# Kernel optimization log

Measured on AMD Instinct MI355X. Metric: run time of the kernel, lower is better.

Reference implementation:

```python
import jax, jax.numpy as jnp
import numpy as np


def setup_inputs() -> dict:
    key = jax.random.key(0)
    B, S, H, D = 4, 2048, 16, 64
    kq, kk, kv, kl = jax.random.split(key, 4)
    q = jax.random.normal(kq, (B, S, H, D), dtype=jnp.float32)
    k = jax.random.normal(kk, (B, S, H, D), dtype=jnp.float32)
    v = jax.random.normal(kv, (B, S, H, D), dtype=jnp.float32)
    # varlen: each sequence has a valid prefix length in [S//2, S]
    lengths = jax.random.randint(kl, (B,), S // 2, S + 1)
    key_padding_mask = jnp.arange(S)[None, :] < lengths[:, None]  # [B, S] bool
    return {"q": q, "k": k, "v": v, "key_padding_mask": key_padding_mask}


def reference(q, k, v, key_padding_mask):
    # q,k,v: [B, S, H, D]; key_padding_mask: [B, S] (True = valid key/value token).
    # Equivalent math of ring varlen flash attention: every query attends to all
    # valid (unpadded) key positions of its sequence; padded keys are excluded.
    D = q.shape[-1]
    scale = 1.0 / np.sqrt(D).astype(np.float32)
    scores = jnp.einsum('bshd,bthd->bhst', q, k) * scale  # [B, H, S, S]
    neg = jnp.finfo(scores.dtype).min
    scores = jnp.where(key_padding_mask[:, None, None, :], scores, neg)
    probs = jax.nn.softmax(scores, axis=-1)
    context = jnp.einsum('bhst,bthd->bshd', probs, v)  # [B, S, H, D]
    return context
```

## Files before the change

### kernel.cpp

```cpp
#include <hip/hip_runtime.h>

#define BB 4
#define SS 2048
#define HH 16
#define DD 64

#define NQW 4
#define QW  32
#define QB  (NQW*QW)
#define KVB 32

#define KRS 144
#define VRS 72

typedef short bf16x8 __attribute__((ext_vector_type(8)));
typedef float f32x16 __attribute__((ext_vector_type(16)));

__device__ __forceinline__ unsigned cvtpk(float lo, float hi){
    unsigned r;
    asm("v_cvt_pk_bf16_f32 %0, %1, %2" : "=v"(r) : "v"(lo), "v"(hi));
    return r;
}

#if __has_builtin(__builtin_amdgcn_exp2f)
#define EXP2F(x) __builtin_amdgcn_exp2f(x)
#else
__device__ __forceinline__ float exp2_asm(float x){
    float r; asm("v_exp_f32 %0, %1\n\ts_nop 0" : "=v"(r) : "v"(x)); return r;
}
#define EXP2F(x) exp2_asm(x)
#endif

union FragU { unsigned u[4]; bf16x8 v; };

#if __has_builtin(__builtin_amdgcn_permlane32_swap)
__device__ __forceinline__ void plswap(unsigned &a, unsigned &b, int ){
    auto r = __builtin_amdgcn_permlane32_swap(a, b, false, false);
    a = r[0]; b = r[1];
}
#else
__device__ __forceinline__ void plswap(unsigned &a, unsigned &b, int lh){
    unsigned sb = (unsigned)__shfl_xor((int)b, 32);
    unsigned sa = (unsigned)__shfl_xor((int)a, 32);
    unsigned na = lh ? sb : a;
    unsigned nb = lh ? b  : sa;
    a = na; b = nb;
}
#endif

__global__ __launch_bounds__(256)
void attn_mfma(const float* __restrict__ qg, const float* __restrict__ kg,
               const float* __restrict__ vg, const int* __restrict__ maskg,
               float* __restrict__ outg)
{
    __shared__ __align__(16) unsigned char kl_raw[2][KVB*KRS];
    __shared__ __align__(16) unsigned char vt_raw[2][DD*VRS];
    __shared__ int lsum_s[NQW];

    const int i0 = (int)blockIdx.x;
    const int x  = i0 & 7;
    const int j  = i0 >> 3;
    const int qt = j & 15;
    const int g  = j >> 4;
    const int b  = (x + g) & 3;
    const int h  = (g << 1) | (x >> 2);

    const int t    = (int)threadIdx.x;
    const int wid  = t >> 6;
    const int lane = t & 63;
    const int lq   = lane & 31;
    const int lh   = lane >> 5;

    const int* mrow = maskg + b*SS;
    int part = 0;
    #pragma unroll
    for (int i = 0; i < 8; ++i) part += mrow[t*8 + i];
    #pragma unroll
    for (int off = 1; off < 64; off <<= 1) part += __shfl_xor(part, off);
    if (lane == 0) lsum_s[wid] = part;
    __syncthreads();
    const int L  = lsum_s[0] + lsum_s[1] + lsum_s[2] + lsum_s[3];
    const int nt = (L + KVB - 1) / KVB;

    const int q0 = qt*QB + wid*QW + lq;
    const float* qrow = qg + ((size_t)((size_t)b*SS + q0)*HH + h)*DD;
    const float QSC = 0.125f * 1.44269504088896340736f;
    bf16x8 Qh[4];
    #pragma unroll
    for (int kc = 0; kc < 4; ++kc) {
        const float* p = qrow + kc*16 + lh*8;
        float4 a = *(const float4*)p;
        float4 c4 = *(const float4*)(p + 4);
        FragU f;
        f.u[0] = cvtpk(a.x*QSC, a.y*QSC);
        f.u[1] = cvtpk(a.z*QSC, a.w*QSC);
        f.u[2] = cvtpk(c4.x*QSC, c4.y*QSC);
        f.u[3] = cvtpk(c4.z*QSC, c4.w*QSC);
        Qh[kc] = f.v;
    }

    f32x16 O0, O1;
    #pragma unroll
    for (int i = 0; i < 16; ++i) { O0[i] = 0.f; O1[i] = 0.f; }
    float lp = 0.f;

    const size_t kvstride = (size_t)HH*DD;
    const float* kbase = kg + ((size_t)b*SS*HH + h)*(size_t)DD;
    const float* vbase = vg + ((size_t)b*SS*HH + h)*(size_t)DD;

    const int skr  = t >> 3;
    const int sc8  = (t & 7) * 8;
    const int skp  = t & 15;
    const int d0v  = (t >> 4) * 4;

    float kx[8], va_[4], vb_[4];

    auto LOADT = [&](int kt0) {
        const float* kp = kbase + (size_t)(kt0 + skr)*kvstride + sc8;
        float4 a = *(const float4*)kp;  float4 c4 = *(const float4*)(kp + 4);
        kx[0]=a.x; kx[1]=a.y; kx[2]=a.z; kx[3]=a.w;
        kx[4]=c4.x; kx[5]=c4.y; kx[6]=c4.z; kx[7]=c4.w;
        const float* vp0 = vbase + (size_t)(kt0 + 2*skp)*kvstride + d0v;
        const float* vp1 = vp0 + kvstride;
        float4 d4 = *(const float4*)vp0;
        float4 e4 = *(const float4*)vp1;
        va_[0]=d4.x; va_[1]=d4.y; va_[2]=d4.z; va_[3]=d4.w;
        vb_[0]=e4.x; vb_[1]=e4.y; vb_[2]=e4.z; vb_[3]=e4.w;
    };

    auto CVTW = [&](int bsel) {
        FragU kf;
        #pragma unroll
        for (int jj = 0; jj < 4; ++jj) kf.u[jj] = cvtpk(kx[2*jj], kx[2*jj+1]);
        unsigned koff = (unsigned)skr*KRS + (unsigned)sc8*2u;
        koff ^= ((unsigned)(skr>>3)&3u) << 4;
        *(bf16x8*)(kl_raw[bsel] + koff) = kf.v;
        #pragma unroll
        for (int i2 = 0; i2 < 4; ++i2) {
            unsigned dw = cvtpk(va_[i2], vb_[i2]);
            *(unsigned*)(vt_raw[bsel] + (unsigned)(d0v + i2)*VRS + (unsigned)skp*4u) = dw;
        }
    };

    LOADT(0);
    CVTW(0);

    for (int it = 0; it < nt; ++it) {
        __syncthreads();
        const int  cur  = it & 1;
        const bool more = (it + 1 < nt);
        if (more) LOADT((it + 1) * KVB);

        f32x16 S;
        #pragma unroll
        for (int i = 0; i < 16; ++i) S[i] = 0.f;
        __builtin_amdgcn_s_setprio(1);
        #pragma unroll
        for (int kc = 0; kc < 4; ++kc) {
            unsigned off = (unsigned)lq*KRS + (unsigned)(kc*32 + lh*16);
            off ^= ((unsigned)(lq>>3)&3u) << 4;
            FragU kf;
            kf.v = *(const bf16x8*)(kl_raw[cur] + off);
            S = __builtin_amdgcn_mfma_f32_32x32x16_bf16(kf.v, Qh[kc], S, 0, 0, 0);
        }
        __builtin_amdgcn_s_setprio(0);

        const int kt0 = it * KVB;
        if (kt0 + KVB > L) {
            #pragma unroll
            for (int r = 0; r < 16; ++r) {
                const int key = kt0 + (r&3) + 8*(r>>2) + 4*lh;
                if (key >= L) S[r] = -1e30f;
            }
        }

        float p[16];
        #pragma unroll
        for (int r = 0; r < 16; ++r) p[r] = EXP2F(S[r]);

        float s0 = (p[0] + p[1]) + (p[2] + p[3]);
        float s1 = (p[4] + p[5]) + (p[6] + p[7]);
        float s2 = (p[8] + p[9]) + (p[10] + p[11]);
        float s3 = (p[12] + p[13]) + (p[14] + p[15]);
        lp += (s0 + s1) + (s2 + s3);

        unsigned dw[8];
        #pragma unroll
        for (int jj = 0; jj < 8; ++jj) dw[jj] = cvtpk(p[2*jj], p[2*jj+1]);
        plswap(dw[0], dw[2], lh);  plswap(dw[1], dw[3], lh);
        plswap(dw[4], dw[6], lh);  plswap(dw[5], dw[7], lh);
        FragU B0, B1;
        B0.u[0]=dw[0]; B0.u[1]=dw[1]; B0.u[2]=dw[2]; B0.u[3]=dw[3];
        B1.u[0]=dw[4]; B1.u[1]=dw[5]; B1.u[2]=dw[6]; B1.u[3]=dw[7];

        const unsigned char* vtb = vt_raw[cur];
        __builtin_amdgcn_s_setprio(1);
        #pragma unroll
        for (int kc = 0; kc < 2; ++kc) {
            const unsigned ko = (unsigned)(kc*32 + lh*16);
            FragU vva, vvb;
            *(uint2*)&vva.u[0] = *(const uint2*)(vtb + (unsigned)lq*VRS + ko);
            *(uint2*)&vva.u[2] = *(const uint2*)(vtb + (unsigned)lq*VRS + ko + 8);
            *(uint2*)&vvb.u[0] = *(const uint2*)(vtb + (unsigned)(lq+32)*VRS + ko);
            *(uint2*)&vvb.u[2] = *(const uint2*)(vtb + (unsigned)(lq+32)*VRS + ko + 8);
            O0 = __builtin_amdgcn_mfma_f32_32x32x16_bf16(vva.v, kc ? B1.v : B0.v, O0, 0, 0, 0);
            O1 = __builtin_amdgcn_mfma_f32_32x32x16_bf16(vvb.v, kc ? B1.v : B0.v, O1, 0, 0, 0);
        }
        __builtin_amdgcn_s_setprio(0);

        if (more) CVTW(cur ^ 1);
    }

    lp += __shfl_xor(lp, 32);
    const float inv = 1.0f / lp;
    float* orow = outg + ((size_t)((size_t)b*SS + q0)*HH + h)*DD;
    #pragma unroll
    for (int run = 0; run < 4; ++run) {
        float4 w0, w1;
        w0.x = O0[4*run+0]*inv; w0.y = O0[4*run+1]*inv;
        w0.z = O0[4*run+2]*inv; w0.w = O0[4*run+3]*inv;
        w1.x = O1[4*run+0]*inv; w1.y = O1[4*run+1]*inv;
        w1.z = O1[4*run+2]*inv; w1.w = O1[4*run+3]*inv;
        *(float4*)(orow + 8*run + 4*lh)      = w0;
        *(float4*)(orow + 32 + 8*run + 4*lh) = w1;
    }
}

extern "C" void kernel_launch(void* const* d_in, const int* in_sizes, int n_in,
                              void* d_out, int out_size, void* d_ws, size_t ws_size,
                              hipStream_t stream) {
    const float* q    = (const float*)d_in[0];
    const float* k    = (const float*)d_in[1];
    const float* v    = (const float*)d_in[2];
    const int*   mask = (const int*)d_in[3];
    float* out = (float*)d_out;

    dim3 grid(BB * HH * (SS / QB));
    dim3 block(256);
    hipLaunchKernelGGL(attn_mfma, grid, block, 0, stream, q, k, v, mask, out);
}
```

Measured before the change: 91.16 us.

## Process two 32-query sub-tiles per wave and permute K rows to drop permlane swaps

Each wave now handles 64 queries as two 32-row halves that share the same K and V fragments read from LDS. The block covers 256 queries, so the grid is halved. The K rows are permuted when written to LDS so that the exp'd score layout directly matches the B operand of the PV MFMA, which removes the permlane32 swaps. V fragments are loaded as full 16-byte reads at the top of the iteration, with VRS changed to 80. This roughly halves the per-query LDS traffic and K/V global loads, but it raises register pressure and leaves fewer blocks to fill the CUs.

```diff
diff --git a/kernel.cpp b/kernel.cpp
--- a/kernel.cpp
+++ b/kernel.cpp
@@ -6,12 +6,12 @@
 #define DD 64
 
 #define NQW 4
-#define QW  32
+#define QW  64
 #define QB  (NQW*QW)
 #define KVB 32
 
 #define KRS 144
-#define VRS 72
+#define VRS 80
 
 typedef short bf16x8 __attribute__((ext_vector_type(8)));
 typedef float f32x16 __attribute__((ext_vector_type(16)));
@@ -32,21 +32,6 @@
 #endif
 
 union FragU { unsigned u[4]; bf16x8 v; };
-
-#if __has_builtin(__builtin_amdgcn_permlane32_swap)
-__device__ __forceinline__ void plswap(unsigned &a, unsigned &b, int ){
-    auto r = __builtin_amdgcn_permlane32_swap(a, b, false, false);
-    a = r[0]; b = r[1];
-}
-#else
-__device__ __forceinline__ void plswap(unsigned &a, unsigned &b, int lh){
-    unsigned sb = (unsigned)__shfl_xor((int)b, 32);
-    unsigned sa = (unsigned)__shfl_xor((int)a, 32);
-    unsigned na = lh ? sb : a;
-    unsigned nb = lh ? b  : sa;
-    a = na; b = nb;
-}
-#endif
 
 __global__ __launch_bounds__(256)
 void attn_mfma(const float* __restrict__ qg, const float* __restrict__ kg,
@@ -60,8 +45,8 @@
     const int i0 = (int)blockIdx.x;
     const int x  = i0 & 7;
     const int j  = i0 >> 3;
-    const int qt = j & 15;
-    const int g  = j >> 4;
+    const int qt = j & 7;
+    const int g  = j >> 3;
     const int b  = (x + g) & 3;
     const int h  = (g << 1) | (x >> 2);
 
@@ -82,27 +67,37 @@
     const int L  = lsum_s[0] + lsum_s[1] + lsum_s[2] + lsum_s[3];
     const int nt = (L + KVB - 1) / KVB;
 
-    const int q0 = qt*QB + wid*QW + lq;
-    const float* qrow = qg + ((size_t)((size_t)b*SS + q0)*HH + h)*DD;
+    const int qA = qt*QB + wid*QW + lq;
+    const float* qrowA = qg + ((size_t)((size_t)b*SS + qA)*HH + h)*DD;
+    const float* qrowB = qrowA + (size_t)32*HH*DD;
     const float QSC = 0.125f * 1.44269504088896340736f;
-    bf16x8 Qh[4];
+    bf16x8 QhA[4], QhB[4];
     #pragma unroll
     for (int kc = 0; kc < 4; ++kc) {
-        const float* p = qrow + kc*16 + lh*8;
-        float4 a = *(const float4*)p;
-        float4 c4 = *(const float4*)(p + 4);
-        FragU f;
-        f.u[0] = cvtpk(a.x*QSC, a.y*QSC);
-        f.u[1] = cvtpk(a.z*QSC, a.w*QSC);
-        f.u[2] = cvtpk(c4.x*QSC, c4.y*QSC);
-        f.u[3] = cvtpk(c4.z*QSC, c4.w*QSC);
-        Qh[kc] = f.v;
+        const float* pa = qrowA + kc*16 + lh*8;
+        float4 a0 = *(const float4*)pa;
+        float4 a1 = *(const float4*)(pa + 4);
+        FragU fa;
+        fa.u[0] = cvtpk(a0.x*QSC, a0.y*QSC);
+        fa.u[1] = cvtpk(a0.z*QSC, a0.w*QSC);
+        fa.u[2] = cvtpk(a1.x*QSC, a1.y*QSC);
+        fa.u[3] = cvtpk(a1.z*QSC, a1.w*QSC);
+        QhA[kc] = fa.v;
+        const float* pb = qrowB + kc*16 + lh*8;
+        float4 b0 = *(const float4*)pb;
+        float4 b1 = *(const float4*)(pb + 4);
+        FragU fb;
+        fb.u[0] = cvtpk(b0.x*QSC, b0.y*QSC);
+        fb.u[1] = cvtpk(b0.z*QSC, b0.w*QSC);
+        fb.u[2] = cvtpk(b1.x*QSC, b1.y*QSC);
+        fb.u[3] = cvtpk(b1.z*QSC, b1.w*QSC);
+        QhB[kc] = fb.v;
     }
 
-    f32x16 O0, O1;
-    #pragma unroll
-    for (int i = 0; i < 16; ++i) { O0[i] = 0.f; O1[i] = 0.f; }
-    float lp = 0.f;
+    f32x16 OA0, OA1, OB0, OB1, ZERO;
+    #pragma unroll
+    for (int i = 0; i < 16; ++i) { OA0[i]=0.f; OA1[i]=0.f; OB0[i]=0.f; OB1[i]=0.f; ZERO[i]=0.f; }
+    float lpA = 0.f, lpB = 0.f;
 
     const size_t kvstride = (size_t)HH*DD;
     const float* kbase = kg + ((size_t)b*SS*HH + h)*(size_t)DD;
@@ -110,6 +105,8 @@
 
     const int skr  = t >> 3;
     const int sc8  = (t & 7) * 8;
+    const int blkp = ((skr >> 2) ^ (skr >> 3)) & 1;
+    const int pskr = skr ^ (blkp ? 12 : 0);
     const int skp  = t & 15;
     const int d0v  = (t >> 4) * 4;
 
@@ -132,8 +129,8 @@
         FragU kf;
         #pragma unroll
         for (int jj = 0; jj < 4; ++jj) kf.u[jj] = cvtpk(kx[2*jj], kx[2*jj+1]);
-        unsigned koff = (unsigned)skr*KRS + (unsigned)sc8*2u;
-        koff ^= ((unsigned)(skr>>3)&3u) << 4;
+        unsigned koff = (unsigned)pskr*KRS + (unsigned)sc8*2u;
+        koff ^= ((unsigned)(pskr>>3)&3u) << 4;
         *(bf16x8*)(kl_raw[bsel] + koff) = kf.v;
         #pragma unroll
         for (int i2 = 0; i2 < 4; ++i2) {
@@ -149,19 +146,31 @@
         __syncthreads();
         const int  cur  = it & 1;
         const bool more = (it + 1 < nt);
+
+        const unsigned char* vtb = vt_raw[cur];
+        FragU v00, v10, v01, v11;
+        v00.v = *(const bf16x8*)(vtb + (unsigned)lq*VRS + (unsigned)(lh*16));
+        v10.v = *(const bf16x8*)(vtb + (unsigned)(lq+32)*VRS + (unsigned)(lh*16));
+        v01.v = *(const bf16x8*)(vtb + (unsigned)lq*VRS + (unsigned)(32 + lh*16));
+        v11.v = *(const bf16x8*)(vtb + (unsigned)(lq+32)*VRS + (unsigned)(32 + lh*16));
+
         if (more) LOADT((it + 1) * KVB);
 
-        f32x16 S;
-        #pragma unroll
-        for (int i = 0; i < 16; ++i) S[i] = 0.f;
-        __builtin_amdgcn_s_setprio(1);
+        const unsigned char* klb = kl_raw[cur];
+        FragU kfr[4];
         #pragma unroll
         for (int kc = 0; kc < 4; ++kc) {
             unsigned off = (unsigned)lq*KRS + (unsigned)(kc*32 + lh*16);
             off ^= ((unsigned)(lq>>3)&3u) << 4;
-            FragU kf;
-            kf.v = *(const bf16x8*)(kl_raw[cur] + off);
-            S = __builtin_amdgcn_mfma_f32_32x32x16_bf16(kf.v, Qh[kc], S, 0, 0, 0);
+            kfr[kc].v = *(const bf16x8*)(klb + off);
+        }
+        __builtin_amdgcn_s_setprio(1);
+        f32x16 SA = __builtin_amdgcn_mfma_f32_32x32x16_bf16(kfr[0].v, QhA[0], ZERO, 0, 0, 0);
+        f32x16 SB = __builtin_amdgcn_mfma_f32_32x32x16_bf16(kfr[0].v, QhB[0], ZERO, 0, 0, 0);
+        #pragma unroll
+        for (int kc = 1; kc < 4; ++kc) {
+            SA = __builtin_amdgcn_mfma_f32_32x32x16_bf16(kfr[kc].v, QhA[kc], SA, 0, 0, 0);
+            SB = __builtin_amdgcn_mfma_f32_32x32x16_bf16(kfr[kc].v, QhB[kc], SB, 0, 0, 0);
         }
         __builtin_amdgcn_s_setprio(0);
 
@@ -169,60 +178,73 @@
         if (kt0 + KVB > L) {
             #pragma unroll
             for (int r = 0; r < 16; ++r) {
-                const int key = kt0 + (r&3) + 8*(r>>2) + 4*lh;
-                if (key >= L) S[r] = -1e30f;
+                const int key = kt0 + r + 8*(r>>3) + 8*lh;
+                if (key >= L) { SA[r] = -1e30f; SB[r] = -1e30f; }
             }
         }
 
-        float p[16];
-        #pragma unroll
-        for (int r = 0; r < 16; ++r) p[r] = EXP2F(S[r]);
-
-        float s0 = (p[0] + p[1]) + (p[2] + p[3]);
-        float s1 = (p[4] + p[5]) + (p[6] + p[7]);
-        float s2 = (p[8] + p[9]) + (p[10] + p[11]);
-        float s3 = (p[12] + p[13]) + (p[14] + p[15]);
-        lp += (s0 + s1) + (s2 + s3);
-
-        unsigned dw[8];
-        #pragma unroll
-        for (int jj = 0; jj < 8; ++jj) dw[jj] = cvtpk(p[2*jj], p[2*jj+1]);
-        plswap(dw[0], dw[2], lh);  plswap(dw[1], dw[3], lh);
-        plswap(dw[4], dw[6], lh);  plswap(dw[5], dw[7], lh);
-        FragU B0, B1;
-        B0.u[0]=dw[0]; B0.u[1]=dw[1]; B0.u[2]=dw[2]; B0.u[3]=dw[3];
-        B1.u[0]=dw[4]; B1.u[1]=dw[5]; B1.u[2]=dw[6]; B1.u[3]=dw[7];
-
-        const unsigned char* vtb = vt_raw[cur];
+        float pA[16], pB[16];
+        #pragma unroll
+        for (int r = 0; r < 16; ++r) pA[r] = EXP2F(SA[r]);
+        #pragma unroll
+        for (int r = 0; r < 16; ++r) pB[r] = EXP2F(SB[r]);
+
+        float a0 = (pA[0]+pA[1]) + (pA[2]+pA[3]);
+        float a1 = (pA[4]+pA[5]) + (pA[6]+pA[7]);
+        float a2 = (pA[8]+pA[9]) + (pA[10]+pA[11]);
+        float a3 = (pA[12]+pA[13]) + (pA[14]+pA[15]);
+        lpA += (a0 + a1) + (a2 + a3);
+        float b0s = (pB[0]+pB[1]) + (pB[2]+pB[3]);
+        float b1s = (pB[4]+pB[5]) + (pB[6]+pB[7]);
+        float b2s = (pB[8]+pB[9]) + (pB[10]+pB[11]);
+        float b3s = (pB[12]+pB[13]) + (pB[14]+pB[15]);
+        lpB += (b0s + b1s) + (b2s + b3s);
+
+        FragU BA0, BA1, BB0, BB1;
+        BA0.u[0]=cvtpk(pA[0],pA[1]);   BA0.u[1]=cvtpk(pA[2],pA[3]);
+        BA0.u[2]=cvtpk(pA[4],pA[5]);   BA0.u[3]=cvtpk(pA[6],pA[7]);
+        BA1.u[0]=cvtpk(pA[8],pA[9]);   BA1.u[1]=cvtpk(pA[10],pA[11]);
+        BA1.u[2]=cvtpk(pA[12],pA[13]); BA1.u[3]=cvtpk(pA[14],pA[15]);
+        BB0.u[0]=cvtpk(pB[0],pB[1]);   BB0.u[1]=cvtpk(pB[2],pB[3]);
+        BB0.u[2]=cvtpk(pB[4],pB[5]);   BB0.u[3]=cvtpk(pB[6],pB[7]);
+        BB1.u[0]=cvtpk(pB[8],pB[9]);   BB1.u[1]=cvtpk(pB[10],pB[11]);
+        BB1.u[2]=cvtpk(pB[12],pB[13]); BB1.u[3]=cvtpk(pB[14],pB[15]);
+
         __builtin_amdgcn_s_setprio(1);
-        #pragma unroll
-        for (int kc = 0; kc < 2; ++kc) {
-            const unsigned ko = (unsigned)(kc*32 + lh*16);
-            FragU vva, vvb;
-            *(uint2*)&vva.u[0] = *(const uint2*)(vtb + (unsigned)lq*VRS + ko);
-            *(uint2*)&vva.u[2] = *(const uint2*)(vtb + (unsigned)lq*VRS + ko + 8);
-            *(uint2*)&vvb.u[0] = *(const uint2*)(vtb + (unsigned)(lq+32)*VRS + ko);
-            *(uint2*)&vvb.u[2] = *(const uint2*)(vtb + (unsigned)(lq+32)*VRS + ko + 8);
-            O0 = __builtin_amdgcn_mfma_f32_32x32x16_bf16(vva.v, kc ? B1.v : B0.v, O0, 0, 0, 0);
-            O1 = __builtin_amdgcn_mfma_f32_32x32x16_bf16(vvb.v, kc ? B1.v : B0.v, O1, 0, 0, 0);
-        }
+        OA0 = __builtin_amdgcn_mfma_f32_32x32x16_bf16(v00.v, BA0.v, OA0, 0, 0, 0);
+        OA1 = __builtin_amdgcn_mfma_f32_32x32x16_bf16(v10.v, BA0.v, OA1, 0, 0, 0);
+        OB0 = __builtin_amdgcn_mfma_f32_32x32x16_bf16(v00.v, BB0.v, OB0, 0, 0, 0);
+        OB1 = __builtin_amdgcn_mfma_f32_32x32x16_bf16(v10.v, BB0.v, OB1, 0, 0, 0);
+        OA0 = __builtin_amdgcn_mfma_f32_32x32x16_bf16(v01.v, BA1.v, OA0, 0, 0, 0);
+        OA1 = __builtin_amdgcn_mfma_f32_32x32x16_bf16(v11.v, BA1.v, OA1, 0, 0, 0);
+        OB0 = __builtin_amdgcn_mfma_f32_32x32x16_bf16(v01.v, BB1.v, OB0, 0, 0, 0);
+        OB1 = __builtin_amdgcn_mfma_f32_32x32x16_bf16(v11.v, BB1.v, OB1, 0, 0, 0);
         __builtin_amdgcn_s_setprio(0);
 
         if (more) CVTW(cur ^ 1);
     }
 
-    lp += __shfl_xor(lp, 32);
-    const float inv = 1.0f / lp;
-    float* orow = outg + ((size_t)((size_t)b*SS + q0)*HH + h)*DD;
+    lpA += __shfl_xor(lpA, 32);
+    lpB += __shfl_xor(lpB, 32);
+    const float invA = 1.0f / lpA;
+    const float invB = 1.0f / lpB;
+    float* orowA = outg + ((size_t)((size_t)b*SS + qA)*HH + h)*DD;
+    float* orowB = orowA + (size_t)32*HH*DD;
     #pragma unroll
     for (int run = 0; run < 4; ++run) {
         float4 w0, w1;
-        w0.x = O0[4*run+0]*inv; w0.y = O0[4*run+1]*inv;
-        w0.z = O0[4*run+2]*inv; w0.w = O0[4*run+3]*inv;
-        w1.x = O1[4*run+0]*inv; w1.y = O1[4*run+1]*inv;
-        w1.z = O1[4*run+2]*inv; w1.w = O1[4*run+3]*inv;
-        *(float4*)(orow + 8*run + 4*lh)      = w0;
-        *(float4*)(orow + 32 + 8*run + 4*lh) = w1;
+        w0.x = OA0[4*run+0]*invA; w0.y = OA0[4*run+1]*invA;
+        w0.z = OA0[4*run+2]*invA; w0.w = OA0[4*run+3]*invA;
+        w1.x = OA1[4*run+0]*invA; w1.y = OA1[4*run+1]*invA;
+        w1.z = OA1[4*run+2]*invA; w1.w = OA1[4*run+3]*invA;
+        *(float4*)(orowA + 8*run + 4*lh)      = w0;
+        *(float4*)(orowA + 32 + 8*run + 4*lh) = w1;
+        w0.x = OB0[4*run+0]*invB; w0.y = OB0[4*run+1]*invB;
+        w0.z = OB0[4*run+2]*invB; w0.w = OB0[4*run+3]*invB;
+        w1.x = OB1[4*run+0]*invB; w1.y = OB1[4*run+1]*invB;
+        w1.z = OB1[4*run+2]*invB; w1.w = OB1[4*run+3]*invB;
+        *(float4*)(orowB + 8*run + 4*lh)      = w0;
+        *(float4*)(orowB + 32 + 8*run + 4*lh) = w1;
     }
 }
 
```

Result: no change. 92.58 us (+1.6%).
